# Kernel optimization log

Measured on AMD Instinct MI355X. Metric: run time of the kernel, lower is better.

Reference implementation:

```python
import jax, jax.numpy as jnp
import numpy as np
from jax import lax

K = 3  # neighbors, as in torch_geometric.nn.knn_interpolate default
EPS = 1e-16


def knn_interpolate(x, pos_x, pos_y):
    """Interpolate features x defined at pos_x onto query points pos_y.
    x: [Ns, F], pos_x: [Ns, 3], pos_y: [Nq, 3] -> [Nq, F].
    Inverse squared-distance weighting over K nearest neighbors."""
    # squared distances via the |y|^2 + |x|^2 - 2 y.x expansion (no [Nq,Ns,3] temp)
    d2 = (jnp.sum(pos_y * pos_y, -1, keepdims=True)
          + jnp.sum(pos_x * pos_x, -1)[None, :]
          - 2.0 * pos_y @ pos_x.T)                      # [Nq, Ns]
    neg_d2, idx = lax.top_k(-d2, K)                      # [Nq, K]
    w = 1.0 / jnp.clip(-neg_d2, EPS)                     # inverse squared distance
    w = w / jnp.sum(w, -1, keepdims=True)
    return jnp.einsum('qk,qkf->qf', w, x[idx])           # gather + weighted reduce


def mlp(x, W1, b1, W2, b2, W3, b3):
    x = jax.nn.relu(x @ W1 + b1)
    x = jax.nn.relu(x @ W2 + b2)
    return x @ W3 + b3


def setup_inputs() -> dict:
    key = jax.random.key(0)
    ks = jax.random.split(key, 16)
    Nh, Nl, H, O = 16384, 4096, 256, 3
    s = lambda fan: 1.0 / np.sqrt(fan)
    return {
        'emb1':  jax.random.normal(ks[0], (Nh, H), jnp.float32),
        'l_y1':  jax.random.normal(ks[1], (Nl, O), jnp.float32),
        'l_pos1': jax.random.uniform(ks[2], (Nl, 3), jnp.float32),
        'h_pos1': jax.random.uniform(ks[3], (Nh, 3), jnp.float32),
        'emb2':  jax.random.normal(ks[4], (Nh, H), jnp.float32),
        'l_y2':  jax.random.normal(ks[5], (Nl, O), jnp.float32),
        'l_pos2': jax.random.uniform(ks[6], (Nl, 3), jnp.float32),
        'h_pos2': jax.random.uniform(ks[7], (Nh, 3), jnp.float32),
        'W1': jax.random.uniform(ks[8], (H, H), jnp.float32, -s(H), s(H)),
        'b1': jax.random.uniform(ks[9], (H,), jnp.float32, -s(H), s(H)),
        'W2': jax.random.uniform(ks[10], (H, H), jnp.float32, -s(H), s(H)),
        'b2': jax.random.uniform(ks[11], (H,), jnp.float32, -s(H), s(H)),
        'W3': jax.random.uniform(ks[12], (H, O), jnp.float32, -s(H), s(H)),
        'b3': jax.random.uniform(ks[13], (O,), jnp.float32, -s(H), s(H)),
    }


def reference(emb1, l_y1, l_pos1, h_pos1, emb2, l_y2, l_pos2, h_pos2,
              W1, b1, W2, b2, W3, b3):
    x = mlp(emb1 - knn_interpolate(emb2, h_pos2, h_pos1), W1, b1, W2, b2, W3, b3)
    # residual=True branch
    res = knn_interpolate(l_y1 - knn_interpolate(l_y2, l_pos2, l_pos1), l_pos1, h_pos1)
    return x + res
```

## Files before the change

kernel.cpp:

```cpp
#include <hip/hip_runtime.h>
#include <math.h>

#define BIGF 3.0e38f

typedef short  s16x8 __attribute__((ext_vector_type(8)));
typedef float  f32x4 __attribute__((ext_vector_type(4)));

__device__ __forceinline__ unsigned short f2bf(float x) {
  unsigned int b = __float_as_uint(x);
  unsigned int r = b + 0x7FFFu + ((b >> 16) & 1u);
  return (unsigned short)(r >> 16);
}
__device__ __forceinline__ float bf2f(unsigned short h) {
  return __uint_as_float(((unsigned int)h) << 16);
}


__device__ __forceinline__ int cell_clamp(float v, int G) {
  int c = (int)(v * (float)G);
  return min(G - 1, max(0, c));
}

__device__ __forceinline__ void ins3(float d, int id,
                                     float& d0, float& d1, float& d2,
                                     int& i0, int& i1, int& i2) {
  bool l0 = (d < d0) || (d == d0 && id < i0);
  bool l1 = (d < d1) || (d == d1 && id < i1);
  bool l2 = (d < d2) || (d == d2 && id < i2);
  float nd0 = l0 ? d  : d0;  int ni0 = l0 ? id : i0;
  float nd1 = l0 ? d0 : (l1 ? d  : d1);
  int   ni1 = l0 ? i0 : (l1 ? id : i1);
  float nd2 = l1 ? d1 : (l2 ? d  : d2);
  int   ni2 = l1 ? i1 : (l2 ? id : i2);
  d0 = nd0; d1 = nd1; d2 = nd2; i0 = ni0; i1 = ni1; i2 = ni2;
}

__device__ __forceinline__ void scan_shell(
    int R, int sl, int G, int cx, int cy, int cz,
    const int* __restrict__ offs, const float4* __restrict__ spts,
    const int* __restrict__ sidx,
    float qx, float qy, float qz, float sy,
    float& d0, float& d1, float& d2v, int& i0, int& i1, int& i2)
{
  #pragma clang fp contract(off)
  #define DIST_INS(SV, IDV)                                                   \
    { float p0 = qx * SV.x, p1 = qy * SV.y, p2 = qz * SV.z;                   \
      float dt = (p0 + p1) + p2;                                              \
      float S  = sy + SV.w;                                                   \
      float dd = S - 2.0f * dt;                                               \
      ins3(dd, IDV, d0, d1, d2v, i0, i1, i2); }

  #define SCANP()                                                             \
    { int j = js;                                                             \
      for (; j + 4 <= je; j += 4) {                                           \
        float4 s0 = spts[j],     s1 = spts[j + 1];                            \
        float4 s2 = spts[j + 2], s3 = spts[j + 3];                            \
        int id0 = sidx[j],     id1 = sidx[j + 1];                             \
        int id2 = sidx[j + 2], id3 = sidx[j + 3];                             \
        DIST_INS(s0, id0) DIST_INS(s1, id1)                                   \
        DIST_INS(s2, id2) DIST_INS(s3, id3)                                   \
      }                                                                       \
      for (; j < je; ++j) {                                                   \
        float4 s = spts[j]; int id = sidx[j];                                 \
        DIST_INS(s, id)                                                       \
      } }

  if (R == 1) {
    if (sl < 9) {
      int dy = sl % 3 - 1, dz = sl / 3 - 1;
      int yy = cy + dy, zz = cz + dz;
      if (yy >= 0 && yy < G && zz >= 0 && zz < G) {
        int xs = max(cx - 1, 0), xe = min(cx + 1, G - 1);
        int base = (zz * G + yy) * G;
        int js = offs[base + xs], je = offs[base + xe + 1];
        SCANP()
      }
    }
  } else {
    const int twoR1 = 2 * R + 1, inner = 2 * R - 1;
    const int nfz = 2 * twoR1;
    const int nfull = nfz + 2 * inner;
    const int half = inner * inner;
    const int nitems = nfull + 2 * half;
    for (int m = sl; m < nitems; m += 16) {
      int dy, dz, js, je;
      if (m < nfull) {
        if (m < nfz) { dz = (m < twoR1) ? -R : R; dy = (m % twoR1) - R; }
        else { int u = m - nfz; dy = (u < inner) ? -R : R; dz = (u % inner) - (R - 1); }
        int yy = cy + dy, zz = cz + dz;
        if (yy < 0 || yy >= G || zz < 0 || zz >= G) continue;
        int xs = max(cx - R, 0), xe = min(cx + R, G - 1);
        int base = (zz * G + yy) * G;
        js = offs[base + xs]; je = offs[base + xe + 1];
      } else {
        int u = m - nfull;
        int xc = (u < half) ? (cx - R) : (cx + R);
        int r2 = (u < half) ? u : u - half;
        dy = r2 % inner - (R - 1); dz = r2 / inner - (R - 1);
        int yy = cy + dy, zz = cz + dz;
        if (xc < 0 || xc >= G || yy < 0 || yy >= G || zz < 0 || zz >= G) continue;
        int c = (zz * G + yy) * G + xc;
        js = offs[c]; je = offs[c + 1];
      }
      SCANP()
    }
  }
  #undef SCANP
  #undef DIST_INS
}

#define MERGE16(E0, E1, E2, J0, J1, J2)                                       \
  { _Pragma("unroll")                                                         \
    for (int msk = 1; msk < 16; msk <<= 1) {                                  \
      float o0 = __shfl_xor(E0, msk), o1 = __shfl_xor(E1, msk), o2 = __shfl_xor(E2, msk); \
      int   p0 = __shfl_xor(J0, msk), p1 = __shfl_xor(J1, msk), p2 = __shfl_xor(J2, msk); \
      ins3(o0, p0, E0, E1, E2, J0, J1, J2);                                   \
      ins3(o1, p1, E0, E1, E2, J0, J1, J2);                                   \
      ins3(o2, p2, E0, E1, E2, J0, J1, J2);                                   \
    } }

__device__ __forceinline__ void knn_search(
    int sl, float qx, float qy, float qz, float sy, int G,
    const int* __restrict__ offs, const float4* __restrict__ spts,
    const int* __restrict__ sidx,
    float& e0, float& e1, float& e2, int& j0, int& j1, int& j2)
{
  const float cs = 1.0f / (float)G;
  const int cx = cell_clamp(qx, G), cy = cell_clamp(qy, G), cz = cell_clamp(qz, G);
  float d0 = BIGF, d1 = BIGF, d2v = BIGF;
  int i0 = -1, i1 = -1, i2 = -1;
  bool done = false;
  for (int R = 1; R <= G; ++R) {
    if (!done) {
      scan_shell(R, sl, G, cx, cy, cz, offs, spts, sidx,
                 qx, qy, qz, sy, d0, d1, d2v, i0, i1, i2);
      e0 = d0; e1 = d1; e2 = d2v; j0 = i0; j1 = i1; j2 = i2;
      MERGE16(e0, e1, e2, j0, j1, j2)
      float bnd = (float)R * cs;
      done = (e2 <= bnd * bnd - 1e-6f) || (R >= G);
    }
    if (__all(done)) break;
  }
}

__device__ void knn0_bt_body(
    int bid,
    const float4* __restrict__ qspts, const int* __restrict__ qsidx, int Nq,
    int G, const int* __restrict__ offs, const float4* __restrict__ spts, const int* __restrict__ sidx,
    const float* __restrict__ emb1, const float* __restrict__ emb2,
    unsigned short* __restrict__ t_hi, unsigned short* __restrict__ t_lo)
{
  const int sl = threadIdx.x & 15;
  const int qs = bid * 8 + (threadIdx.x >> 4);
  if (qs >= Nq) return;
  float4 qv = qspts[qs];
  const int qorig = qsidx[qs];

  float e0, e1, e2; int j0, j1, j2;
  knn_search(sl, qv.x, qv.y, qv.z, qv.w, G, offs, spts, sidx,
             e0, e1, e2, j0, j1, j2);

  float w0 = 1.0f / fmaxf(e0, 1e-16f);
  float w1 = 1.0f / fmaxf(e1, 1e-16f);
  float w2 = 1.0f / fmaxf(e2, 1e-16f);
  float inv = 1.0f / (w0 + w1 + w2);
  w0 *= inv; w1 *= inv; w2 *= inv;
  const float4* e1p = (const float4*)emb1;
  const float4* e2p = (const float4*)emb2;
  #pragma unroll
  for (int k = 0; k < 4; ++k) {
    int c4 = sl + 16 * k;
    float4 a  = e1p[(size_t)qorig * 64 + c4];
    float4 f0 = e2p[(size_t)j0 * 64 + c4];
    float4 f1 = e2p[(size_t)j1 * 64 + c4];
    float4 f2 = e2p[(size_t)j2 * 64 + c4];
    float4 r;
    r.x = a.x - (w0 * f0.x + w1 * f1.x + w2 * f2.x);
    r.y = a.y - (w0 * f0.y + w1 * f1.y + w2 * f2.y);
    r.z = a.z - (w0 * f0.z + w1 * f1.z + w2 * f2.z);
    r.w = a.w - (w0 * f0.w + w1 * f1.w + w2 * f2.w);
    ushort4 h, l;
    h.x = f2bf(r.x); l.x = f2bf(r.x - bf2f(h.x));
    h.y = f2bf(r.y); l.y = f2bf(r.y - bf2f(h.y));
    h.z = f2bf(r.z); l.z = f2bf(r.z - bf2f(h.z));
    h.w = f2bf(r.w); l.w = f2bf(r.w - bf2f(h.w));
    size_t o = (size_t)qorig * 256 + (size_t)c4 * 4;
    *(ushort4*)&t_hi[o] = h;
    *(ushort4*)&t_lo[o] = l;
  }
}

__device__ void knn2_body(
    int bid,
    const float4* __restrict__ qspts, const int* __restrict__ qsidx, int Nq,
    int G, const int* __restrict__ offs, const float4* __restrict__ spts, const int* __restrict__ sidx,
    float* __restrict__ wC_out, int* __restrict__ iC_out)
{
  const int sl = threadIdx.x & 15;
  const int qs = bid * 8 + (threadIdx.x >> 4);
  if (qs >= Nq) return;
  float4 qv = qspts[qs];
  const int qorig = qsidx[qs];

  float e0, e1, e2; int j0, j1, j2;
  knn_search(sl, qv.x, qv.y, qv.z, qv.w, G, offs, spts, sidx,
             e0, e1, e2, j0, j1, j2);

  if (sl == 0) {
    float w0 = 1.0f / fmaxf(e0, 1e-16f);
    float w1 = 1.0f / fmaxf(e1, 1e-16f);
    float w2 = 1.0f / fmaxf(e2, 1e-16f);
    float inv = 1.0f / (w0 + w1 + w2);
    wC_out[(size_t)qorig * 3 + 0] = w0 * inv;
    wC_out[(size_t)qorig * 3 + 1] = w1 * inv;
    wC_out[(size_t)qorig * 3 + 2] = w2 * inv;
    iC_out[(size_t)qorig * 3 + 0] = j0;
    iC_out[(size_t)qorig * 3 + 1] = j1;
    iC_out[(size_t)qorig * 3 + 2] = j2;
  }
}

__device__ void knn1_body(
    int bid,
    const float4* __restrict__ qspts, const int* __restrict__ qsidx, int Nq, int G,
    const int* __restrict__ offs, const float4* __restrict__ spts, const int* __restrict__ sidx,
    const float* __restrict__ base3, const float* __restrict__ feat3,
    float* __restrict__ out3)
{
  const int sl = threadIdx.x & 15;
  const int qs = bid * 8 + (threadIdx.x >> 4);
  if (qs >= Nq) return;
  float4 qv = qspts[qs];
  const int qorig = qsidx[qs];

  float e0, e1, e2; int j0, j1, j2;
  knn_search(sl, qv.x, qv.y, qv.z, qv.w, G, offs, spts, sidx,
             e0, e1, e2, j0, j1, j2);

  if (sl == 0) {
    float w0 = 1.0f / fmaxf(e0, 1e-16f);
    float w1 = 1.0f / fmaxf(e1, 1e-16f);
    float w2 = 1.0f / fmaxf(e2, 1e-16f);
    float inv = 1.0f / (w0 + w1 + w2);
    w0 *= inv; w1 *= inv; w2 *= inv;
    #pragma unroll
    for (int f = 0; f < 3; ++f) {
      float v = w0 * feat3[(size_t)j0 * 3 + f]
              + w1 * feat3[(size_t)j1 * 3 + f]
              + w2 * feat3[(size_t)j2 * 3 + f];
      out3[(size_t)qorig * 3 + f] = base3[(size_t)qorig * 3 + f] - v;
    }
  }
}

__device__ void res_gather_body(
    int bid, const float* __restrict__ wC, const int* __restrict__ idxC,
    const float* __restrict__ diff, float* __restrict__ res, int Nq)
{
  int q = bid * 256 + threadIdx.x;
  if (q >= Nq) return;
  float w0 = wC[(size_t)q * 3 + 0], w1 = wC[(size_t)q * 3 + 1], w2 = wC[(size_t)q * 3 + 2];
  int i0 = idxC[(size_t)q * 3 + 0], i1 = idxC[(size_t)q * 3 + 1], i2 = idxC[(size_t)q * 3 + 2];
  #pragma unroll
  for (int f = 0; f < 3; ++f) {
    res[(size_t)q * 3 + f] = w0 * diff[(size_t)i0 * 3 + f]
                           + w1 * diff[(size_t)i1 * 3 + f]
                           + w2 * diff[(size_t)i2 * 3 + f];
  }
}

__global__ __launch_bounds__(128) void knn_all_kernel(
    const float4* qspts, const int* qsidx, int Nh,
    int G1, const int* offs1, const float4* spts1, const int* sidx1,
    const float* emb1, const float* emb2,
    unsigned short* t_hi, unsigned short* t_lo,
    int G2, const int* offs3, const float4* spts3, const int* sidx3,
    float* wC, int* idxC,
    int Nl, const int* offs2, const float4* spts2, const int* sidx2,
    const float* l_y1, const float* l_y2, float* diff)
{
  int g = blockIdx.x / 9, r = blockIdx.x % 9;
  if (r < 4)
    knn0_bt_body(g * 4 + r, qspts, qsidx, Nh, G1, offs1, spts1, sidx1,
                 emb1, emb2, t_hi, t_lo);
  else if (r < 8)
    knn2_body(g * 4 + (r - 4), qspts, qsidx, Nh, G2, offs3, spts3, sidx3,
              wC, idxC);
  else
    knn1_body(g, spts3, sidx3, Nl, G2, offs2, spts2, sidx2,
              l_y1, l_y2, diff);
}

__global__ __launch_bounds__(256) void zero_kernel(int* __restrict__ p, int n) {
  int i = blockIdx.x * 256 + threadIdx.x;
  if (i < n) p[i] = 0;
}

__global__ __launch_bounds__(256) void count_split_kernel(
    const float* __restrict__ p1, int n1, int g1, int* __restrict__ c1,
    const float* __restrict__ p2, int n2, int g2, int* __restrict__ c2,
    const float* __restrict__ p3, int n3, int g3, int* __restrict__ c3,
    const float* __restrict__ p4, int n4, int g4, int* __restrict__ c4,
    const float* __restrict__ W1, unsigned short* __restrict__ h1T, unsigned short* __restrict__ l1T,
    const float* __restrict__ W2, unsigned short* __restrict__ h2T, unsigned short* __restrict__ l2T)
{
  int b = blockIdx.x;
  if (b >= 160) {
    int sb = b - 160;
    const float* W = (sb < 256) ? W1 : W2;
    unsigned short* hiT = (sb < 256) ? h1T : h2T;
    unsigned short* loT = (sb < 256) ? l1T : l2T;
    int id = (sb & 255) * 256 + threadIdx.x;
    int k = id >> 8, n = id & 255;
    float x = W[id];
    unsigned short h = f2bf(x);
    unsigned short l = f2bf(x - bf2f(h));
    hiT[n * 256 + k] = h;
    loT[n * 256 + k] = l;
    return;
  }
  const float* p; int n, G; int* cnt; int i;
  if (b < 64)       { p = p1; n = n1; G = g1; cnt = c1; i = b * 256 + threadIdx.x; }
  else if (b < 80)  { p = p2; n = n2; G = g2; cnt = c2; i = (b - 64) * 256 + threadIdx.x; }
  else if (b < 96)  { p = p3; n = n3; G = g3; cnt = c3; i = (b - 80) * 256 + threadIdx.x; }
  else              { p = p4; n = n4; G = g4; cnt = c4; i = (b - 96) * 256 + threadIdx.x; }
  if (i >= n) return;
  int cx = cell_clamp(p[3 * i],     G);
  int cy = cell_clamp(p[3 * i + 1], G);
  int cz = cell_clamp(p[3 * i + 2], G);
  atomicAdd(&cnt[(cz * G + cy) * G + cx], 1);
}

__global__ __launch_bounds__(256) void prefix4_kernel(
    const int* __restrict__ c1, int* __restrict__ o1, int* __restrict__ u1, int m1,
    const int* __restrict__ c2, int* __restrict__ o2, int* __restrict__ u2, int m2,
    const int* __restrict__ c3, int* __restrict__ o3, int* __restrict__ u3, int m3,
    const int* __restrict__ c4, int* __restrict__ o4, int* __restrict__ u4, int m4)
{
  const int* cnt; int* offs; int* cur; int M;
  if (blockIdx.x == 0)      { cnt = c1; offs = o1; cur = u1; M = m1; }
  else if (blockIdx.x == 1) { cnt = c2; offs = o2; cur = u2; M = m2; }
  else if (blockIdx.x == 2) { cnt = c3; offs = o3; cur = u3; M = m3; }
  else                      { cnt = c4; offs = o4; cur = u4; M = m4; }
  __shared__ int ps[256];
  const int tid = threadIdx.x;
  const int per = (M + 255) >> 8;
  const int base = tid * per;
  int s = 0;
  for (int j = 0; j < per; ++j) if (base + j < M) s += cnt[base + j];
  ps[tid] = s;
  __syncthreads();
  for (int off = 1; off < 256; off <<= 1) {
    int v = (tid >= off) ? ps[tid - off] : 0;
    __syncthreads();
    ps[tid] += v;
    __syncthreads();
  }
  int run = (tid > 0) ? ps[tid - 1] : 0;
  for (int j = 0; j < per; ++j) {
    if (base + j < M) {
      offs[base + j] = run; cur[base + j] = run;
      run += cnt[base + j];
    }
  }
  if (tid == 255) offs[M] = run;
}

__global__ __launch_bounds__(256) void scatter4_kernel(
    const float* __restrict__ p1, int n1, int g1, int* __restrict__ u1, float4* __restrict__ s1, int* __restrict__ x1,
    const float* __restrict__ p2, int n2, int g2, int* __restrict__ u2, float4* __restrict__ s2, int* __restrict__ x2,
    const float* __restrict__ p3, int n3, int g3, int* __restrict__ u3, float4* __restrict__ s3, int* __restrict__ x3,
    const float* __restrict__ p4, int n4, int g4, int* __restrict__ u4, float4* __restrict__ s4, int* __restrict__ x4)
{
  #pragma clang fp contract(off)
  int b = blockIdx.x;
  const float* p; int n, G; int* cur; float4* spts; int* sidx; int i;
  if (b < 64)       { p = p1; n = n1; G = g1; cur = u1; spts = s1; sidx = x1; i = b * 256 + threadIdx.x; }
  else if (b < 80)  { p = p2; n = n2; G = g2; cur = u2; spts = s2; sidx = x2; i = (b - 64) * 256 + threadIdx.x; }
  else if (b < 96)  { p = p3; n = n3; G = g3; cur = u3; spts = s3; sidx = x3; i = (b - 80) * 256 + threadIdx.x; }
  else              { p = p4; n = n4; G = g4; cur = u4; spts = s4; sidx = x4; i = (b - 96) * 256 + threadIdx.x; }
  if (i >= n) return;
  float x = p[3 * i], y = p[3 * i + 1], z = p[3 * i + 2];
  int cx = cell_clamp(x, G), cy = cell_clamp(y, G), cz = cell_clamp(z, G);
  int c = (cz * G + cy) * G + cx;
  int pos = atomicAdd(&cur[c], 1);
  float sx = (x * x + y * y) + z * z;
  spts[pos] = make_float4(x, y, z, sx);
  sidx[pos] = i;
}

__global__ __launch_bounds__(256) void mfma_gemm_kernel(
    const unsigned short* __restrict__ A_hi, const unsigned short* __restrict__ A_lo,
    const unsigned short* __restrict__ BT_hi, const unsigned short* __restrict__ BT_lo,
    const float* __restrict__ bias,
    float* __restrict__ outf,
    unsigned short* __restrict__ out_hi, unsigned short* __restrict__ out_lo,
    int relu, int split_out, int ngemm,
    const float* __restrict__ wC, const int* __restrict__ idxC,
    const float* __restrict__ diff, float* __restrict__ resout, int NqG)
{
  __shared__ unsigned short Bs_hi[64][132];
  __shared__ unsigned short Bs_lo[64][132];
  const int t = threadIdx.x;
  const int d = blockIdx.x;
  if (d >= ngemm) {
    res_gather_body(d - ngemm, wC, idxC, diff, resout, NqG);
    return;
  }
  const int xcd = d & 7, slot = d >> 3;
  const int lin = xcd * (ngemm >> 3) + slot;
  const int row0 = (lin >> 2) * 64;
  const int col0 = (lin & 3) * 64;

  const int l = t & 63, w = t >> 6;
  const int lr = l & 15;
  const int lk = (l >> 4) << 3;
  const unsigned short* arh = A_hi + (size_t)(row0 + w * 16 + lr) * 256;
  const unsigned short* arl = A_lo + (size_t)(row0 + w * 16 + lr) * 256;

  const int sc = t >> 2;
  const int sk = (t & 3) << 5;

  f32x4 acc0 = {0.f,0.f,0.f,0.f}, acc1 = {0.f,0.f,0.f,0.f};
  f32x4 acc2 = {0.f,0.f,0.f,0.f}, acc3 = {0.f,0.f,0.f,0.f};

  #define KSTEP(CT, ACC)                                                      \
    { s16x8 bh = *(const s16x8*)&Bs_hi[CT * 16 + lr][kc + lk];                \
      s16x8 bl = *(const s16x8*)&Bs_lo[CT * 16 + lr][kc + lk];                \
      ACC = __builtin_amdgcn_mfma_f32_16x16x32_bf16(ah, bh, ACC, 0, 0, 0);    \
      ACC = __builtin_amdgcn_mfma_f32_16x16x32_bf16(al, bh, ACC, 0, 0, 0);    \
      ACC = __builtin_amdgcn_mfma_f32_16x16x32_bf16(ah, bl, ACC, 0, 0, 0); }

  for (int half = 0; half < 2; ++half) {
    if (half) __syncthreads();
    {
      const int4* sh = (const int4*)&BT_hi[(size_t)(col0 + sc) * 256 + half * 128 + sk];
      const int4* slo = (const int4*)&BT_lo[(size_t)(col0 + sc) * 256 + half * 128 + sk];
      int4* dh = (int4*)&Bs_hi[sc][sk];
      int4* dl = (int4*)&Bs_lo[sc][sk];
      #pragma unroll
      for (int i = 0; i < 4; ++i) { dh[i] = sh[i]; dl[i] = slo[i]; }
    }
    __syncthreads();
    const int kbase = half * 128;
    #pragma unroll
    for (int kc = 0; kc < 128; kc += 32) {
      s16x8 ah = *(const s16x8*)&arh[kbase + kc + lk];
      s16x8 al = *(const s16x8*)&arl[kbase + kc + lk];
      KSTEP(0, acc0)
      KSTEP(1, acc1)
      KSTEP(2, acc2)
      KSTEP(3, acc3)
    }
  }
  #undef KSTEP

  const int orow = row0 + w * 16 + ((l >> 4) << 2);
  #define EPILOG(CT, ACC)                                                     \
    { int col = col0 + CT * 16 + lr;                                          \
      float bb = bias[col];                                                   \
      _Pragma("unroll")                                                       \
      for (int r = 0; r < 4; ++r) {                                           \
        float v = ACC[r] + bb;                                                \
        if (relu) v = fmaxf(v, 0.0f);                                         \
        size_t o = (size_t)(orow + r) * 256 + col;                            \
        if (split_out) {                                                      \
          unsigned short hh = f2bf(v);                                        \
          out_hi[o] = hh; out_lo[o] = f2bf(v - bf2f(hh));                     \
        } else {                                                              \
          outf[o] = v;                                                        \
        }                                                                     \
      } }
  EPILOG(0, acc0)
  EPILOG(1, acc1)
  EPILOG(2, acc2)
  EPILOG(3, acc3)
  #undef EPILOG
}

__global__ __launch_bounds__(256) void final_kernel(
    const float* __restrict__ h2, const float* __restrict__ W3,
    const float* __restrict__ b3, const float* __restrict__ res,
    float* __restrict__ out, int M)
{
  __shared__ float sW3[768];
  const int tid = threadIdx.x;
  for (int i = tid; i < 768; i += 256) sW3[i] = W3[i];
  __syncthreads();

  const int wave = tid >> 6, lane = tid & 63;
  const int r = blockIdx.x * 4 + wave;
  if (r >= M) return;

  float4 h = ((const float4*)h2)[(size_t)r * 64 + lane];
  const int c = lane * 4;
  float a0 = h.x * sW3[(c + 0) * 3 + 0] + h.y * sW3[(c + 1) * 3 + 0]
           + h.z * sW3[(c + 2) * 3 + 0] + h.w * sW3[(c + 3) * 3 + 0];
  float a1 = h.x * sW3[(c + 0) * 3 + 1] + h.y * sW3[(c + 1) * 3 + 1]
           + h.z * sW3[(c + 2) * 3 + 1] + h.w * sW3[(c + 3) * 3 + 1];
  float a2 = h.x * sW3[(c + 0) * 3 + 2] + h.y * sW3[(c + 1) * 3 + 2]
           + h.z * sW3[(c + 2) * 3 + 2] + h.w * sW3[(c + 3) * 3 + 2];

  #pragma unroll
  for (int off = 32; off; off >>= 1) {
    a0 += __shfl_xor(a0, off);
    a1 += __shfl_xor(a1, off);
    a2 += __shfl_xor(a2, off);
  }
  if (lane == 0) {
    out[(size_t)r * 3 + 0] = a0 + b3[0] + res[(size_t)r * 3 + 0];
    out[(size_t)r * 3 + 1] = a1 + b3[1] + res[(size_t)r * 3 + 1];
    out[(size_t)r * 3 + 2] = a2 + b3[2] + res[(size_t)r * 3 + 2];
  }
}

extern "C" void kernel_launch(void* const* d_in, const int* in_sizes, int n_in,
                              void* d_out, int out_size, void* d_ws, size_t ws_size,
                              hipStream_t stream) {
  (void)in_sizes; (void)n_in; (void)out_size; (void)ws_size;
  const float* emb1   = (const float*)d_in[0];
  const float* l_y1   = (const float*)d_in[1];
  const float* l_pos1 = (const float*)d_in[2];
  const float* h_pos1 = (const float*)d_in[3];
  const float* emb2   = (const float*)d_in[4];
  const float* l_y2   = (const float*)d_in[5];
  const float* l_pos2 = (const float*)d_in[6];
  const float* h_pos2 = (const float*)d_in[7];
  const float* W1     = (const float*)d_in[8];
  const float* b1     = (const float*)d_in[9];
  const float* W2     = (const float*)d_in[10];
  const float* b2     = (const float*)d_in[11];
  const float* W3     = (const float*)d_in[12];
  const float* b3     = (const float*)d_in[13];
  float* out = (float*)d_out;

  const int Nh = 16384, Nl = 4096, H = 256;
  const int G1 = 16, G2 = 10;
  const int M1 = G1 * G1 * G1, M2 = G2 * G2 * G2;

  char* wsp = (char*)d_ws;
  size_t off = 0;
  auto alloc = [&](size_t bytes) -> void* {
    void* p = wsp + off;
    off += (bytes + 255) & ~(size_t)255;
    return p;
  };
  int*            idxC   = (int*)           alloc((size_t)Nh * 3 * 4);
  float*          wC     = (float*)         alloc((size_t)Nh * 3 * 4);
  unsigned short* t_hi   = (unsigned short*)alloc((size_t)Nh * H * 2);
  unsigned short* t_lo   = (unsigned short*)alloc((size_t)Nh * H * 2);
  unsigned short* h1_hi  = (unsigned short*)alloc((size_t)Nh * H * 2);
  unsigned short* h1_lo  = (unsigned short*)alloc((size_t)Nh * H * 2);
  float*          h2     = (float*)t_hi;
  unsigned short* w1t_hi = (unsigned short*)alloc((size_t)H * H * 2);
  unsigned short* w1t_lo = (unsigned short*)alloc((size_t)H * H * 2);
  unsigned short* w2t_hi = (unsigned short*)alloc((size_t)H * H * 2);
  unsigned short* w2t_lo = (unsigned short*)alloc((size_t)H * H * 2);
  float*          diff   = (float*)         alloc((size_t)Nl * 3 * 4);
  float*          res    = (float*)         alloc((size_t)Nh * 3 * 4);
  int*            cnts   = (int*)           alloc((size_t)(M1 + M2 + M2 + M1) * 4);
  int* cnt1 = cnts, *cnt2 = cnts + M1, *cnt3 = cnts + M1 + M2, *cnt4 = cnts + M1 + 2 * M2;
  int*            offs1  = (int*)           alloc((size_t)(M1 + 1) * 4);
  int*            cur1   = (int*)           alloc((size_t)M1 * 4);
  int*            offs2  = (int*)           alloc((size_t)(M2 + 1) * 4);
  int*            cur2   = (int*)           alloc((size_t)M2 * 4);
  int*            offs3  = (int*)           alloc((size_t)(M2 + 1) * 4);
  int*            cur3   = (int*)           alloc((size_t)M2 * 4);
  int*            offs4  = (int*)           alloc((size_t)(M1 + 1) * 4);
  int*            cur4   = (int*)           alloc((size_t)M1 * 4);
  float4*         spts1  = (float4*)        alloc((size_t)Nh * 16);
  int*            sidx1  = (int*)           alloc((size_t)Nh * 4);
  float4*         spts2  = (float4*)        alloc((size_t)Nl * 16);
  int*            sidx2  = (int*)           alloc((size_t)Nl * 4);
  float4*         spts3  = (float4*)        alloc((size_t)Nl * 16);
  int*            sidx3  = (int*)           alloc((size_t)Nl * 4);
  float4*         qspts  = (float4*)        alloc((size_t)Nh * 16);
  int*            qsidx  = (int*)           alloc((size_t)Nh * 4);

  const int ncnt = M1 + M2 + M2 + M1;
  zero_kernel<<<(ncnt + 255) / 256, 256, 0, stream>>>(cnts, ncnt);
  count_split_kernel<<<672, 256, 0, stream>>>(
      h_pos2, Nh, G1, cnt1,  l_pos2, Nl, G2, cnt2,
      l_pos1, Nl, G2, cnt3,  h_pos1, Nh, G1, cnt4,
      W1, w1t_hi, w1t_lo, W2, w2t_hi, w2t_lo);
  prefix4_kernel<<<4, 256, 0, stream>>>(
      cnt1, offs1, cur1, M1,  cnt2, offs2, cur2, M2,
      cnt3, offs3, cur3, M2,  cnt4, offs4, cur4, M1);
  scatter4_kernel<<<160, 256, 0, stream>>>(
      h_pos2, Nh, G1, cur1, spts1, sidx1,
      l_pos2, Nl, G2, cur2, spts2, sidx2,
      l_pos1, Nl, G2, cur3, spts3, sidx3,
      h_pos1, Nh, G1, cur4, qspts, qsidx);

  knn_all_kernel<<<4608, 128, 0, stream>>>(
      qspts, qsidx, Nh,
      G1, offs1, spts1, sidx1, emb1, emb2, t_hi, t_lo,
      G2, offs3, spts3, sidx3, wC, idxC,
      Nl, offs2, spts2, sidx2, l_y1, l_y2, diff);

  mfma_gemm_kernel<<<1024 + 64, 256, 0, stream>>>(
      t_hi, t_lo, w1t_hi, w1t_lo, b1, nullptr, h1_hi, h1_lo, 1, 1, 1024,
      wC, idxC, diff, res, Nh);
  mfma_gemm_kernel<<<1024, 256, 0, stream>>>(
      h1_hi, h1_lo, w2t_hi, w2t_lo, b2, h2, nullptr, nullptr, 1, 0, 1024,
      nullptr, nullptr, nullptr, nullptr, 0);

  final_kernel<<<Nh / 4, 256, 0, stream>>>(h2, W3, b3, res, out, Nh);
}
```

Before: 109.3 us.

## Overlap low-res KNN searches with first GEMM, residual gather with second

Before, a single fused kernel ran all three KNN searches. Now only the high-res embedding KNN runs alone. The second and third KNN searches run as extra blocks appended to the first MLP GEMM launch, with 16 queries per 256-thread block. The residual gather moves into the second GEMM launch. The aim is to hide the independent KNN work behind GEMM compute and shorten the critical path. The risk is that the wider KNN blocks and mixed block types disturb GEMM occupancy or XCD scheduling.

```diff
diff --git a/kernel.cpp b/kernel.cpp
--- a/kernel.cpp
+++ b/kernel.cpp
@@ -143,6 +143,7 @@
   }
 }
 
+template <int QPB>
 __device__ void knn0_bt_body(
     int bid,
     const float4* __restrict__ qspts, const int* __restrict__ qsidx, int Nq,
@@ -151,7 +152,7 @@
     unsigned short* __restrict__ t_hi, unsigned short* __restrict__ t_lo)
 {
   const int sl = threadIdx.x & 15;
-  const int qs = bid * 8 + (threadIdx.x >> 4);
+  const int qs = bid * QPB + (threadIdx.x >> 4);
   if (qs >= Nq) return;
   float4 qv = qspts[qs];
   const int qorig = qsidx[qs];
@@ -190,6 +191,7 @@
   }
 }
 
+template <int QPB>
 __device__ void knn2_body(
     int bid,
     const float4* __restrict__ qspts, const int* __restrict__ qsidx, int Nq,
@@ -197,7 +199,7 @@
     float* __restrict__ wC_out, int* __restrict__ iC_out)
 {
   const int sl = threadIdx.x & 15;
-  const int qs = bid * 8 + (threadIdx.x >> 4);
+  const int qs = bid * QPB + (threadIdx.x >> 4);
   if (qs >= Nq) return;
   float4 qv = qspts[qs];
   const int qorig = qsidx[qs];
@@ -220,6 +222,7 @@
   }
 }
 
+template <int QPB>
 __device__ void knn1_body(
     int bid,
     const float4* __restrict__ qspts, const int* __restrict__ qsidx, int Nq, int G,
@@ -228,7 +231,7 @@
     float* __restrict__ out3)
 {
   const int sl = threadIdx.x & 15;
-  const int qs = bid * 8 + (threadIdx.x >> 4);
+  const int qs = bid * QPB + (threadIdx.x >> 4);
   if (qs >= Nq) return;
   float4 qv = qspts[qs];
   const int qorig = qsidx[qs];
@@ -269,124 +272,14 @@
   }
 }
 
-__global__ __launch_bounds__(128) void knn_all_kernel(
+__global__ __launch_bounds__(128) void knn0_kernel(
     const float4* qspts, const int* qsidx, int Nh,
     int G1, const int* offs1, const float4* spts1, const int* sidx1,
     const float* emb1, const float* emb2,
-    unsigned short* t_hi, unsigned short* t_lo,
-    int G2, const int* offs3, const float4* spts3, const int* sidx3,
-    float* wC, int* idxC,
-    int Nl, const int* offs2, const float4* spts2, const int* sidx2,
-    const float* l_y1, const float* l_y2, float* diff)
-{
-  int g = blockIdx.x / 9, r = blockIdx.x % 9;
-  if (r < 4)
-    knn0_bt_body(g * 4 + r, qspts, qsidx, Nh, G1, offs1, spts1, sidx1,
-                 emb1, emb2, t_hi, t_lo);
-  else if (r < 8)
-    knn2_body(g * 4 + (r - 4), qspts, qsidx, Nh, G2, offs3, spts3, sidx3,
-              wC, idxC);
-  else
-    knn1_body(g, spts3, sidx3, Nl, G2, offs2, spts2, sidx2,
-              l_y1, l_y2, diff);
-}
-
-__global__ __launch_bounds__(256) void zero_kernel(int* __restrict__ p, int n) {
-  int i = blockIdx.x * 256 + threadIdx.x;
-  if (i < n) p[i] = 0;
-}
-
-__global__ __launch_bounds__(256) void count_split_kernel(
-    const float* __restrict__ p1, int n1, int g1, int* __restrict__ c1,
-    const float* __restrict__ p2, int n2, int g2, int* __restrict__ c2,
-    const float* __restrict__ p3, int n3, int g3, int* __restrict__ c3,
-    const float* __restrict__ p4, int n4, int g4, int* __restrict__ c4,
-    const float* __restrict__ W1, unsigned short* __restrict__ h1T, unsigned short* __restrict__ l1T,
-    const float* __restrict__ W2, unsigned short* __restrict__ h2T, unsigned short* __restrict__ l2T)
-{
-  int b = blockIdx.x;
-  if (b >= 160) {
-    int sb = b - 160;
-    const float* W = (sb < 256) ? W1 : W2;
-    unsigned short* hiT = (sb < 256) ? h1T : h2T;
-    unsigned short* loT = (sb < 256) ? l1T : l2T;
-    int id = (sb & 255) * 256 + threadIdx.x;
-    int k = id >> 8, n = id & 255;
-    float x = W[id];
-    unsigned short h = f2bf(x);
-    unsigned short l = f2bf(x - bf2f(h));
-    hiT[n * 256 + k] = h;
-    loT[n * 256 + k] = l;
-    return;
-  }
-  const float* p; int n, G; int* cnt; int i;
-  if (b < 64)       { p = p1; n = n1; G = g1; cnt = c1; i = b * 256 + threadIdx.x; }
-  else if (b < 80)  { p = p2; n = n2; G = g2; cnt = c2; i = (b - 64) * 256 + threadIdx.x; }
-  else if (b < 96)  { p = p3; n = n3; G = g3; cnt = c3; i = (b - 80) * 256 + threadIdx.x; }
-  else              { p = p4; n = n4; G = g4; cnt = c4; i = (b - 96) * 256 + threadIdx.x; }
-  if (i >= n) return;
-  int cx = cell_clamp(p[3 * i],     G);
-  int cy = cell_clamp(p[3 * i + 1], G);
-  int cz = cell_clamp(p[3 * i + 2], G);
-  atomicAdd(&cnt[(cz * G + cy) * G + cx], 1);
-}
-
-__global__ __launch_bounds__(256) void prefix4_kernel(
-    const int* __restrict__ c1, int* __restrict__ o1, int* __restrict__ u1, int m1,
-    const int* __restrict__ c2, int* __restrict__ o2, int* __restrict__ u2, int m2,
-    const int* __restrict__ c3, int* __restrict__ o3, int* __restrict__ u3, int m3,
-    const int* __restrict__ c4, int* __restrict__ o4, int* __restrict__ u4, int m4)
-{
-  const int* cnt; int* offs; int* cur; int M;
-  if (blockIdx.x == 0)      { cnt = c1; offs = o1; cur = u1; M = m1; }
-  else if (blockIdx.x == 1) { cnt = c2; offs = o2; cur = u2; M = m2; }
-  else if (blockIdx.x == 2) { cnt = c3; offs = o3; cur = u3; M = m3; }
-  else                      { cnt = c4; offs = o4; cur = u4; M = m4; }
-  __shared__ int ps[256];
-  const int tid = threadIdx.x;
-  const int per = (M + 255) >> 8;
-  const int base = tid * per;
-  int s = 0;
-  for (int j = 0; j < per; ++j) if (base + j < M) s += cnt[base + j];
-  ps[tid] = s;
-  __syncthreads();
-  for (int off = 1; off < 256; off <<= 1) {
-    int v = (tid >= off) ? ps[tid - off] : 0;
-    __syncthreads();
-    ps[tid] += v;
-    __syncthreads();
-  }
-  int run = (tid > 0) ? ps[tid - 1] : 0;
-  for (int j = 0; j < per; ++j) {
-    if (base + j < M) {
-      offs[base + j] = run; cur[base + j] = run;
-      run += cnt[base + j];
-    }
-  }
-  if (tid == 255) offs[M] = run;
-}
-
-__global__ __launch_bounds__(256) void scatter4_kernel(
-    const float* __restrict__ p1, int n1, int g1, int* __restrict__ u1, float4* __restrict__ s1, int* __restrict__ x1,
-    const float* __restrict__ p2, int n2, int g2, int* __restrict__ u2, float4* __restrict__ s2, int* __restrict__ x2,
-    const float* __restrict__ p3, int n3, int g3, int* __restrict__ u3, float4* __restrict__ s3, int* __restrict__ x3,
-    const float* __restrict__ p4, int n4, int g4, int* __restrict__ u4, float4* __restrict__ s4, int* __restrict__ x4)
-{
-  #pragma clang fp contract(off)
-  int b = blockIdx.x;
-  const float* p; int n, G; int* cur; float4* spts; int* sidx; int i;
-  if (b < 64)       { p = p1; n = n1; G = g1; cur = u1; spts = s1; sidx = x1; i = b * 256 + threadIdx.x; }
-  else if (b < 80)  { p = p2; n = n2; G = g2; cur = u2; spts = s2; sidx = x2; i = (b - 64) * 256 + threadIdx.x; }
-  else if (b < 96)  { p = p3; n = n3; G = g3; cur = u3; spts = s3; sidx = x3; i = (b - 80) * 256 + threadIdx.x; }
-  else              { p = p4; n = n4; G = g4; cur = u4; spts = s4; sidx = x4; i = (b - 96) * 256 + threadIdx.x; }
-  if (i >= n) return;
-  float x = p[3 * i], y = p[3 * i + 1], z = p[3 * i + 2];
-  int cx = cell_clamp(x, G), cy = cell_clamp(y, G), cz = cell_clamp(z, G);
-  int c = (cz * G + cy) * G + cx;
-  int pos = atomicAdd(&cur[c], 1);
-  float sx = (x * x + y * y) + z * z;
-  spts[pos] = make_float4(x, y, z, sx);
-  sidx[pos] = i;
+    unsigned short* t_hi, unsigned short* t_lo)
+{
+  knn0_bt_body<8>(blockIdx.x, qspts, qsidx, Nh, G1, offs1, spts1, sidx1,
+                  emb1, emb2, t_hi, t_lo);
 }
 
 __global__ __launch_bounds__(256) void mfma_gemm_kernel(
@@ -395,16 +288,29 @@
     const float* __restrict__ bias,
     float* __restrict__ outf,
     unsigned short* __restrict__ out_hi, unsigned short* __restrict__ out_lo,
-    int relu, int split_out, int ngemm,
-    const float* __restrict__ wC, const int* __restrict__ idxC,
-    const float* __restrict__ diff, float* __restrict__ resout, int NqG)
+    int relu, int split_out, int ngemm, int variant, int nA,
+    const float4* qspts, const int* qsidx, int Nh,
+    int G2, const int* offs3, const float4* spts3, const int* sidx3,
+    float* wC, int* idxC,
+    int Nl, const int* offs2, const float4* spts2, const int* sidx2,
+    const float* l_y1, const float* l_y2, float* diff,
+    const float* wCr, const int* idxCr, const float* diffr, float* resout, int NqG)
 {
   __shared__ unsigned short Bs_hi[64][132];
   __shared__ unsigned short Bs_lo[64][132];
   const int t = threadIdx.x;
   const int d = blockIdx.x;
   if (d >= ngemm) {
-    res_gather_body(d - ngemm, wC, idxC, diff, resout, NqG);
+    int a = d - ngemm;
+    if (variant == 1) {
+      if (a < nA)
+        knn2_body<16>(a, qspts, qsidx, Nh, G2, offs3, spts3, sidx3, wC, idxC);
+      else
+        knn1_body<16>(a - nA, spts3, sidx3, Nl, G2, offs2, spts2, sidx2,
+                      l_y1, l_y2, diff);
+    } else {
+      res_gather_body(a, wCr, idxCr, diffr, resout, NqG);
+    }
     return;
   }
   const int xcd = d & 7, slot = d >> 3;
@@ -476,6 +382,104 @@
   EPILOG(2, acc2)
   EPILOG(3, acc3)
   #undef EPILOG
+}
+
+__global__ __launch_bounds__(256) void zero_kernel(int* __restrict__ p, int n) {
+  int i = blockIdx.x * 256 + threadIdx.x;
+  if (i < n) p[i] = 0;
+}
+
+__global__ __launch_bounds__(256) void count_split_kernel(
+    const float* __restrict__ p1, int n1, int g1, int* __restrict__ c1,
+    const float* __restrict__ p2, int n2, int g2, int* __restrict__ c2,
+    const float* __restrict__ p3, int n3, int g3, int* __restrict__ c3,
+    const float* __restrict__ p4, int n4, int g4, int* __restrict__ c4,
+    const float* __restrict__ W1, unsigned short* __restrict__ h1T, unsigned short* __restrict__ l1T,
+    const float* __restrict__ W2, unsigned short* __restrict__ h2T, unsigned short* __restrict__ l2T)
+{
+  int b = blockIdx.x;
+  if (b >= 160) {
+    int sb = b - 160;
+    const float* W = (sb < 256) ? W1 : W2;
+    unsigned short* hiT = (sb < 256) ? h1T : h2T;
+    unsigned short* loT = (sb < 256) ? l1T : l2T;
+    int id = (sb & 255) * 256 + threadIdx.x;
+    int k = id >> 8, n = id & 255;
+    float x = W[id];
+    unsigned short h = f2bf(x);
+    unsigned short l = f2bf(x - bf2f(h));
+    hiT[n * 256 + k] = h;
+    loT[n * 256 + k] = l;
+    return;
+  }
+  const float* p; int n, G; int* cnt; int i;
+  if (b < 64)       { p = p1; n = n1; G = g1; cnt = c1; i = b * 256 + threadIdx.x; }
+  else if (b < 80)  { p = p2; n = n2; G = g2; cnt = c2; i = (b - 64) * 256 + threadIdx.x; }
+  else if (b < 96)  { p = p3; n = n3; G = g3; cnt = c3; i = (b - 80) * 256 + threadIdx.x; }
+  else              { p = p4; n = n4; G = g4; cnt = c4; i = (b - 96) * 256 + threadIdx.x; }
+  if (i >= n) return;
+  int cx = cell_clamp(p[3 * i],     G);
+  int cy = cell_clamp(p[3 * i + 1], G);
+  int cz = cell_clamp(p[3 * i + 2], G);
+  atomicAdd(&cnt[(cz * G + cy) * G + cx], 1);
+}
+
+__global__ __launch_bounds__(256) void prefix4_kernel(
+    const int* __restrict__ c1, int* __restrict__ o1, int* __restrict__ u1, int m1,
+    const int* __restrict__ c2, int* __restrict__ o2, int* __restrict__ u2, int m2,
+    const int* __restrict__ c3, int* __restrict__ o3, int* __restrict__ u3, int m3,
+    const int* __restrict__ c4, int* __restrict__ o4, int* __restrict__ u4, int m4)
+{
+  const int* cnt; int* offs; int* cur; int M;
+  if (blockIdx.x == 0)      { cnt = c1; offs = o1; cur = u1; M = m1; }
+  else if (blockIdx.x == 1) { cnt = c2; offs = o2; cur = u2; M = m2; }
+  else if (blockIdx.x == 2) { cnt = c3; offs = o3; cur = u3; M = m3; }
+  else                      { cnt = c4; offs = o4; cur = u4; M = m4; }
+  __shared__ int ps[256];
+  const int tid = threadIdx.x;
+  const int per = (M + 255) >> 8;
+  const int base = tid * per;
+  int s = 0;
+  for (int j = 0; j < per; ++j) if (base + j < M) s += cnt[base + j];
+  ps[tid] = s;
+  __syncthreads();
+  for (int off = 1; off < 256; off <<= 1) {
+    int v = (tid >= off) ? ps[tid - off] : 0;
+    __syncthreads();
+    ps[tid] += v;
+    __syncthreads();
+  }
+  int run = (tid > 0) ? ps[tid - 1] : 0;
+  for (int j = 0; j < per; ++j) {
+    if (base + j < M) {
+      offs[base + j] = run; cur[base + j] = run;
+      run += cnt[base + j];
+    }
+  }
+  if (tid == 255) offs[M] = run;
+}
+
+__global__ __launch_bounds__(256) void scatter4_kernel(
+    const float* __restrict__ p1, int n1, int g1, int* __restrict__ u1, float4* __restrict__ s1, int* __restrict__ x1,
+    const float* __restrict__ p2, int n2, int g2, int* __restrict__ u2, float4* __restrict__ s2, int* __restrict__ x2,
+    const float* __restrict__ p3, int n3, int g3, int* __restrict__ u3, float4* __restrict__ s3, int* __restrict__ x3,
+    const float* __restrict__ p4, int n4, int g4, int* __restrict__ u4, float4* __restrict__ s4, int* __restrict__ x4)
+{
+  #pragma clang fp contract(off)
+  int b = blockIdx.x;
+  const float* p; int n, G; int* cur; float4* spts; int* sidx; int i;
+  if (b < 64)       { p = p1; n = n1; G = g1; cur = u1; spts = s1; sidx = x1; i = b * 256 + threadIdx.x; }
+  else if (b < 80)  { p = p2; n = n2; G = g2; cur = u2; spts = s2; sidx = x2; i = (b - 64) * 256 + threadIdx.x; }
+  else if (b < 96)  { p = p3; n = n3; G = g3; cur = u3; spts = s3; sidx = x3; i = (b - 80) * 256 + threadIdx.x; }
+  else              { p = p4; n = n4; G = g4; cur = u4; spts = s4; sidx = x4; i = (b - 96) * 256 + threadIdx.x; }
+  if (i >= n) return;
+  float x = p[3 * i], y = p[3 * i + 1], z = p[3 * i + 2];
+  int cx = cell_clamp(x, G), cy = cell_clamp(y, G), cz = cell_clamp(z, G);
+  int c = (cz * G + cy) * G + cx;
+  int pos = atomicAdd(&cur[c], 1);
+  float sx = (x * x + y * y) + z * z;
+  spts[pos] = make_float4(x, y, z, sx);
+  sidx[pos] = i;
 }
 
 __global__ __launch_bounds__(256) void final_kernel(
@@ -592,18 +596,23 @@
       l_pos1, Nl, G2, cur3, spts3, sidx3,
       h_pos1, Nh, G1, cur4, qspts, qsidx);
 
-  knn_all_kernel<<<4608, 128, 0, stream>>>(
+  knn0_kernel<<<Nh / 8, 128, 0, stream>>>(
       qspts, qsidx, Nh,
-      G1, offs1, spts1, sidx1, emb1, emb2, t_hi, t_lo,
-      G2, offs3, spts3, sidx3, wC, idxC,
-      Nl, offs2, spts2, sidx2, l_y1, l_y2, diff);
+      G1, offs1, spts1, sidx1, emb1, emb2, t_hi, t_lo);
+
+  mfma_gemm_kernel<<<1024 + 1024 + 256, 256, 0, stream>>>(
+      t_hi, t_lo, w1t_hi, w1t_lo, b1, nullptr, h1_hi, h1_lo, 1, 1,
+      1024, 1, 1024,
+      qspts, qsidx, Nh, G2, offs3, spts3, sidx3, wC, idxC,
+      Nl, offs2, spts2, sidx2, l_y1, l_y2, diff,
+      nullptr, nullptr, nullptr, nullptr, 0);
 
   mfma_gemm_kernel<<<1024 + 64, 256, 0, stream>>>(
-      t_hi, t_lo, w1t_hi, w1t_lo, b1, nullptr, h1_hi, h1_lo, 1, 1, 1024,
+      h1_hi, h1_lo, w2t_hi, w2t_lo, b2, h2, nullptr, nullptr, 1, 0,
+      1024, 0, 64,
+      nullptr, nullptr, 0, 0, nullptr, nullptr, nullptr, nullptr, nullptr,
+      0, nullptr, nullptr, nullptr, nullptr, nullptr, nullptr,
       wC, idxC, diff, res, Nh);
-  mfma_gemm_kernel<<<1024, 256, 0, stream>>>(
-      h1_hi, h1_lo, w2t_hi, w2t_lo, b2, h2, nullptr, nullptr, 1, 0, 1024,
-      nullptr, nullptr, nullptr, nullptr, 0);
 
   final_kernel<<<Nh / 4, 256, 0, stream>>>(h2, W3, b3, res, out, Nh);
 }
```

Result: slower. 126.5 us (+15.7%).
